# Optimization experiments

Measured on AMD Instinct MI355X. Metric: run time of the kernel, lower is better.

## Reference

```python
import jax, jax.numpy as jnp
import numpy as np

N, E, F, C, K, H = 100000, 1600000, 64, 32, 8, 36


def setup_inputs() -> dict:
    key = jax.random.key(0)
    ks = jax.random.split(key, 24)
    s = 0.1
    inp = {
        "x": jax.random.normal(ks[0], (N, F), jnp.float32),
        "edge_index": jax.random.randint(ks[1], (2, E), 0, N, dtype=jnp.int32),
        # ChebConv conv1_1: K x [F, H] weights + bias
        "W1_1": jax.random.normal(ks[2], (K, F, H), jnp.float32) * s,
        "b1_1": jnp.zeros((H,), jnp.float32),
        "g1_1": jnp.ones((H,), jnp.float32),
        "be1_1": jnp.zeros((H,), jnp.float32),
        # ChebConv conv1_2: K x [H, H]
        "W1_2": jax.random.normal(ks[3], (K, H, H), jnp.float32) * s,
        "b1_2": jnp.zeros((H,), jnp.float32),
        "g1_2": jnp.ones((H,), jnp.float32),
        "be1_2": jnp.zeros((H,), jnp.float32),
        # GINConv MLP: Linear(F,H) -> ReLU -> Linear(H,H)
        "gin_w1": jax.random.normal(ks[4], (F, H), jnp.float32) * s,
        "gin_b1": jnp.zeros((H,), jnp.float32),
        "gin_w2": jax.random.normal(ks[5], (H, H), jnp.float32) * s,
        "gin_b2": jnp.zeros((H,), jnp.float32),
        "g2": jnp.ones((H,), jnp.float32),
        "be2": jnp.zeros((H,), jnp.float32),
        # conv4: ChebConv K=1 on concat(3H) -> C  (pure linear, no propagation)
        "W4": jax.random.normal(ks[6], (1, 3 * H, C), jnp.float32) * s,
        "b4": jnp.zeros((C,), jnp.float32),
    }
    return inp


def _spmm(w, src, dst, x, n):
    # out[i] = sum_{e: dst_e=i} w_e * x[src_e]
    return jax.ops.segment_sum(w[:, None] * x[src], dst, num_segments=n)


def _cheb(x, src, dst, w, Wk, b):
    # PyG ChebConv with sym norm, lambda_max=2: L_hat = -D^-1/2 A D^-1/2 (loop weight 0)
    n = x.shape[0]
    Kk = Wk.shape[0]
    Tx0 = x
    out = Tx0 @ Wk[0]
    if Kk > 1:
        Tx1 = _spmm(w, src, dst, Tx0, n)
        out = out + Tx1 @ Wk[1]
        for k in range(2, Kk):
            Tx2 = 2.0 * _spmm(w, src, dst, Tx1, n) - Tx0
            out = out + Tx2 @ Wk[k]
            Tx0, Tx1 = Tx1, Tx2
    return out + b


def _bn(x, g, b, eps=1e-5):
    m = jnp.mean(x, axis=0)
    v = jnp.mean(jnp.square(x - m), axis=0)  # biased var, training-mode BN
    return g * (x - m) * jax.lax.rsqrt(v + eps) + b


def reference(x, edge_index, W1_1, b1_1, g1_1, be1_1, W1_2, b1_2, g1_2, be1_2,
              gin_w1, gin_b1, gin_w2, gin_b2, g2, be2, W4, b4):
    src, dst = edge_index[0], edge_index[1]
    n = x.shape[0]
    deg = jax.ops.segment_sum(jnp.ones((src.shape[0],), x.dtype), src, num_segments=n)
    dis = jnp.where(deg > 0, jax.lax.rsqrt(jnp.maximum(deg, 1.0)), 0.0)
    w = -dis[src] * dis[dst]  # scaled Laplacian edge weights

    x1_1 = jax.nn.relu(_bn(_cheb(x, src, dst, w, W1_1, b1_1), g1_1, be1_1))
    x1_2 = jax.nn.relu(_bn(_cheb(x1_1, src, dst, w, W1_2, b1_2), g1_2, be1_2))

    # GINConv (eps=0): nn(x + sum_{j in N(i)} x_j)
    agg = jax.ops.segment_sum(x[src], dst, num_segments=n)
    h = x + agg
    gin = jax.nn.relu(h @ gin_w1 + gin_b1) @ gin_w2 + gin_b2
    x2 = _bn(jax.nn.relu(gin), g2, be2)

    x4 = jnp.concatenate((x1_1, x1_2, x2), axis=1)
    return x4 @ W4[0] + b4
```

## Files before the change

### kernel.cpp

```cpp
#include <hip/hip_runtime.h>

constexpr int N_NODES = 100000;
constexpr int N_EDGES = 1600000;
constexpr int NBK  = 391;
constexpr int NBLK = 640;
constexpr int CHUNK = 2500;
constexpr int LCNT = NBK * NBLK;
constexpr int SCAN_BLKS = (LCNT + 255) / 256;


__device__ __forceinline__ unsigned bf16pack(float a, float b) {
    unsigned ua = __float_as_uint(a), ub = __float_as_uint(b);
    ua += 0x7fffu + ((ua >> 16) & 1u);
    ub += 0x7fffu + ((ub >> 16) & 1u);
    return (ua >> 16) | (ub & 0xffff0000u);
}
__device__ __forceinline__ float bflo(unsigned p) { return __uint_as_float(p << 16); }
__device__ __forceinline__ float bfhi(unsigned p) { return __uint_as_float(p & 0xffff0000u); }


__global__ __launch_bounds__(256) void part_count_kernel(
    const int* __restrict__ ei, int* __restrict__ cntD, int* __restrict__ cntS) {
    __shared__ int hd[NBK], hs[NBK];
    int tid = threadIdx.x;
    for (int i = tid; i < NBK; i += 256) { hd[i] = 0; hs[i] = 0; }
    __syncthreads();
    int e0 = blockIdx.x * CHUNK;
    for (int e = e0 + tid; e < e0 + CHUNK; e += 256) {
        int s = ei[e], d = ei[N_EDGES + e];
        atomicAdd(&hs[s >> 8], 1);
        atomicAdd(&hd[d >> 8], 1);
    }
    __syncthreads();
    for (int i = tid; i < NBK; i += 256) {
        cntD[i * NBLK + blockIdx.x] = hd[i];
        cntS[i * NBLK + blockIdx.x] = hs[i];
    }
}

__global__ __launch_bounds__(256) void scanA_kernel(const int* __restrict__ in,
                                                    int* __restrict__ out,
                                                    int* __restrict__ bsum, int L) {
    __shared__ int sm[256];
    int i = blockIdx.x * 256 + threadIdx.x;
    int v = (i < L) ? in[i] : 0;
    sm[threadIdx.x] = v;
    __syncthreads();
    for (int off = 1; off < 256; off <<= 1) {
        int t = (threadIdx.x >= off) ? sm[threadIdx.x - off] : 0;
        __syncthreads();
        sm[threadIdx.x] += t;
        __syncthreads();
    }
    if (i < L) out[i] = sm[threadIdx.x] - v;
    if (threadIdx.x == 255) bsum[blockIdx.x] = sm[255];
}

__global__ __launch_bounds__(1024) void scanB_kernel(int* __restrict__ bsum, int nb) {
    __shared__ int sm[1024];
    int t = threadIdx.x;
    int v = (t < nb) ? bsum[t] : 0;
// ... 51 lines not shown
    if (node < N_NODES) dis[node] = cnt[tid] > 0 ? rsqrtf((float)cnt[tid]) : 0.f;
}

__global__ __launch_bounds__(256) void csr_kernel(const int2* __restrict__ edgepart,
                                                  const int* __restrict__ scanD,
                                                  const float* __restrict__ dis,
                                                  int* __restrict__ rp,
                                                  int2* __restrict__ csrw) {
    __shared__ int cnt[256];
    __shared__ int lofs[256];
    __shared__ float disl[256];
    int b = blockIdx.x, tid = threadIdx.x;
    int beg = scanD[b * NBLK];
    int end = (b + 1 < NBK) ? scanD[(b + 1) * NBLK] : N_EDGES;
    int node = b * 256 + tid;
    cnt[tid] = 0;
    disl[tid] = (node < N_NODES) ? dis[node] : 0.f;
    __syncthreads();
    for (int j = beg + tid; j < end; j += 256)
        atomicAdd(&cnt[edgepart[j].y & 255], 1);
    __syncthreads();
    int v = cnt[tid];
    lofs[tid] = v;
    __syncthreads();
    for (int off = 1; off < 256; off <<= 1) {
        int t = (tid >= off) ? lofs[tid - off] : 0;
        __syncthreads();
        lofs[tid] += t;
        __syncthreads();
    }
    int myexc = lofs[tid] - v;
    if (node < N_NODES) rp[node] = beg + myexc;
    if (b == NBK - 1 && tid == 0) rp[N_NODES] = N_EDGES;
    __syncthreads();
    lofs[tid] = myexc;
    cnt[tid] = 0;
    __syncthreads();
    for (int j = beg + tid; j < end; j += 256) {
        int2 e = edgepart[j];
        int dl = e.y & 255;
        int pos = beg + lofs[dl] + atomicAdd(&cnt[dl], 1);
        csrw[pos] = make_int2(e.x, __float_as_int(-dis[e.x] * disl[dl]));
    }
}

__global__ void pack_x_kernel(const float* __restrict__ x, uint2* __restrict__ xbf) {
    int i = blockIdx.x * blockDim.x + threadIdx.x;
    if (i >= N_NODES * 16) return;
    float4 v = ((const float4*)x)[i];
    xbf[i] = make_uint2(bf16pack(v.x, v.y), bf16pack(v.z, v.w));
}


template <int FI, int SCALE, bool HAS_B2, bool BN_A, bool FUSE_STATS, bool OUT_BF16, bool DUAL>
__global__ __launch_bounds__(256) void cheb_step_kernel(
    const int* __restrict__ rp, const int2* __restrict__ csrw,
    const uint2* __restrict__ INb, const uint2* __restrict__ B2b,
    const uint2* __restrict__ Ab, const float* __restrict__ W,
    const float* __restrict__ ss, void* __restrict__ OUT,
    unsigned long long* __restrict__ OUTB, float* __restrict__ partials) {
    constexpr int RU2 = FI / 4;
    __shared__ float Wl[FI * 36];
    __shared__ float Atile[28][FI + 1];
    __shared__ float ls[72];
    int tid = threadIdx.x;
    for (int i = tid; i < FI * 36; i += 252) Wl[i] = W[i];
    int r0 = blockIdx.x * 28;
    const long long* ab8 = (const long long*)Ab;
    for (int i = tid; i < 28 * RU2; i += 252) {
        int r = i / RU2, u = i % RU2;
        int row = r0 + r;
        long long av = (row < N_NODES)
            ? __builtin_nontemporal_load(ab8 + (size_t)row * RU2 + u) : 0LL;
        unsigned lo = (unsigned)av, hi = (unsigned)(av >> 32);
        float f0 = bflo(lo), f1 = bfhi(lo), f2 = bflo(hi), f3 = bfhi(hi);
        if (BN_A) {
            int f = u * 4;
            f0 = fmaxf(fmaf(ss[f + 0], f0, ss[36 + f + 0]), 0.f);
            f1 = fmaxf(fmaf(ss[f + 1], f1, ss[36 + f + 1]), 0.f);
            f2 = fmaxf(fmaf(ss[f + 2], f2, ss[36 + f + 2]), 0.f);
            f3 = fmaxf(fmaf(ss[f + 3], f3, ss[36 + f + 3]), 0.f);
        }
        Atile[r][u * 4 + 0] = f0; Atile[r][u * 4 + 1] = f1;
        Atile[r][u * 4 + 2] = f2; Atile[r][u * 4 + 3] = f3;
    }
    if (FUSE_STATS && tid < 72) ls[tid] = 0.f;
    __syncthreads();
    int r = tid / 9, c = tid % 9;
    int row = r0 + r;
    bool valid = row < N_NODES;
    float ax = 0, ay = 0, az = 0, aw = 0;
    float bx = 0, by = 0, bz = 0, bw = 0;
    float cx = 0, cy = 0, cz = 0, cw = 0;
    float dx = 0, dy = 0, dz = 0, dw = 0;
    if (SCALE != 0 && valid) {
        int beg = rp[row], end = rp[row + 1];
        int j = beg;
        for (; j + 7 < end; j += 8) {
            int2 e0 = csrw[j],     e1 = csrw[j + 1], e2 = csrw[j + 2], e3 = csrw[j + 3];
            int2 e4 = csrw[j + 4], e5 = csrw[j + 5], e6 = csrw[j + 6], e7 = csrw[j + 7];
            uint2 u0 = INb[(size_t)e0.x * 9 + c];
            uint2 u1 = INb[(size_t)e1.x * 9 + c];
            uint2 u2 = INb[(size_t)e2.x * 9 + c];
            uint2 u3 = INb[(size_t)e3.x * 9 + c];
            uint2 u4 = INb[(size_t)e4.x * 9 + c];
            uint2 u5 = INb[(size_t)e5.x * 9 + c];
            uint2 u6 = INb[(size_t)e6.x * 9 + c];
            uint2 u7 = INb[(size_t)e7.x * 9 + c];
            float w0 = __int_as_float(e0.y), w1 = __int_as_float(e1.y);
            float w2 = __int_as_float(e2.y), w3 = __int_as_float(e3.y);
            float w4 = __int_as_float(e4.y), w5 = __int_as_float(e5.y);
            float w6 = __int_as_float(e6.y), w7 = __int_as_float(e7.y);
            ax = fmaf(w0, bflo(u0.x), ax); ay = fmaf(w0, bfhi(u0.x), ay);
            az = fmaf(w0, bflo(u0.y), az); aw = fmaf(w0, bfhi(u0.y), aw);
            bx = fmaf(w1, bflo(u1.x), bx); by = fmaf(w1, bfhi(u1.x), by);
            bz = fmaf(w1, bflo(u1.y), bz); bw = fmaf(w1, bfhi(u1.y), bw);
            cx = fmaf(w2, bflo(u2.x), cx); cy = fmaf(w2, bfhi(u2.x), cy);
            cz = fmaf(w2, bflo(u2.y), cz); cw = fmaf(w2, bfhi(u2.y), cw);
            dx = fmaf(w3, bflo(u3.x), dx); dy = fmaf(w3, bfhi(u3.x), dy);
            dz = fmaf(w3, bflo(u3.y), dz); dw = fmaf(w3, bfhi(u3.y), dw);
            ax = fmaf(w4, bflo(u4.x), ax); ay = fmaf(w4, bfhi(u4.x), ay);
            az = fmaf(w4, bflo(u4.y), az); aw = fmaf(w4, bfhi(u4.y), aw);
            bx = fmaf(w5, bflo(u5.x), bx); by = fmaf(w5, bfhi(u5.x), by);
            bz = fmaf(w5, bflo(u5.y), bz); bw = fmaf(w5, bfhi(u5.y), bw);
            cx = fmaf(w6, bflo(u6.x), cx); cy = fmaf(w6, bfhi(u6.x), cy);
            cz = fmaf(w6, bflo(u6.y), cz); cw = fmaf(w6, bfhi(u6.y), cw);
            dx = fmaf(w7, bflo(u7.x), dx); dy = fmaf(w7, bfhi(u7.x), dy);
            dz = fmaf(w7, bflo(u7.y), dz); dw = fmaf(w7, bfhi(u7.y), dw);
        }
        for (; j < end; ++j) {
            int2 e = csrw[j];
            uint2 u = INb[(size_t)e.x * 9 + c];
            float w = __int_as_float(e.y);
            ax = fmaf(w, bflo(u.x), ax); ay = fmaf(w, bfhi(u.x), ay);
            az = fmaf(w, bflo(u.y), az); aw = fmaf(w, bfhi(u.y), aw);
        }
        ax += bx + cx + dx; ay += by + cy + dy;
        az += bz + cz + dz; aw += bw + cw + dw;
    }
    float px = 0, py = 0, pz = 0, pw = 0;
    const float4* Wl4 = (const float4*)Wl;
#pragma unroll 4
    for (int f = 0; f < FI; ++f) {
        float a = Atile[r][f];
        float4 wv = Wl4[f * 9 + c];
        px = fmaf(a, wv.x, px); py = fmaf(a, wv.y, py);
        pz = fmaf(a, wv.z, pz); pw = fmaf(a, wv.w, pw);
    }
    const float S = (float)SCALE;
    float4 o;
    o.x = fmaf(S, ax, px); o.y = fmaf(S, ay, py);
    o.z = fmaf(S, az, pz); o.w = fmaf(S, aw, pw);
    if (valid) {
        if (HAS_B2) {
            uint2 u = B2b[(size_t)row * 9 + c];
            o.x -= bflo(u.x); o.y -= bfhi(u.x);
            o.z -= bflo(u.y); o.w -= bfhi(u.y);
        }
        if (OUT_BF16) {
            unsigned long long pv = (unsigned long long)bf16pack(o.x, o.y)
                                  | ((unsigned long long)bf16pack(o.z, o.w) << 32);
            __builtin_nontemporal_store(pv, (unsigned long long*)OUT + (size_t)row * 9 + c);
        } else {
            ((float4*)OUT)[(size_t)row * 9 + c] = o;
        }
        if (DUAL) {
            unsigned long long pv = (unsigned long long)bf16pack(o.x, o.y)
                                  | ((unsigned long long)bf16pack(o.z, o.w) << 32);
            __builtin_nontemporal_store(pv, OUTB + (size_t)row * 9 + c);
        }
        if (FUSE_STATS) {
            atomicAdd(&ls[c * 4 + 0], o.x); atomicAdd(&ls[36 + c * 4 + 0], o.x * o.x);
            atomicAdd(&ls[c * 4 + 1], o.y); atomicAdd(&ls[36 + c * 4 + 1], o.y * o.y);
            atomicAdd(&ls[c * 4 + 2], o.z); atomicAdd(&ls[36 + c * 4 + 2], o.z * o.z);
            atomicAdd(&ls[c * 4 + 3], o.w); atomicAdd(&ls[36 + c * 4 + 3], o.w * o.w);
        }
    }
    if (FUSE_STATS) {
        __syncthreads();
        if (tid < 72) partials[blockIdx.x * 72 + tid] = ls[tid];
    }
}


__global__ __launch_bounds__(256) void gin_gather_kernel(
    const int* __restrict__ rp, const int2* __restrict__ csrw,
    const uint2* __restrict__ Yb, const float* __restrict__ b1,
    const float* __restrict__ w2, const float* __restrict__ b2,
    float* __restrict__ OUT, float* __restrict__ partials) {
    __shared__ float W2l[36 * 36];
    __shared__ float B1l[36], B2l[36];
    __shared__ float M1t[28][37];
    __shared__ float ls[72];
    int tid = threadIdx.x;
    for (int i = tid; i < 36 * 36; i += 252) W2l[i] = w2[i];
    if (tid < 36) { B1l[tid] = b1[tid]; B2l[tid] = b2[tid]; }
    if (tid < 72) ls[tid] = 0.f;
    __syncthreads();
    int r = tid / 9, c = tid % 9;
    int row = blockIdx.x * 28 + r;
    bool valid = row < N_NODES;
    float ax = 0, ay = 0, az = 0, aw = 0;
    float bx = 0, by = 0, bz = 0, bw = 0;
    float cx = 0, cy = 0, cz = 0, cw = 0;
    float dx = 0, dy = 0, dz = 0, dw = 0;
    if (valid) {
        uint2 us = Yb[(size_t)row * 9 + c];
        ax = bflo(us.x); ay = bfhi(us.x); az = bflo(us.y); aw = bfhi(us.y);
        int beg = rp[row], end = rp[row + 1];
        int j = beg;
        for (; j + 7 < end; j += 8) {
            int s0 = csrw[j].x,     s1 = csrw[j + 1].x, s2 = csrw[j + 2].x, s3 = csrw[j + 3].x;
            int s4 = csrw[j + 4].x, s5 = csrw[j + 5].x, s6 = csrw[j + 6].x, s7 = csrw[j + 7].x;
            uint2 u0 = Yb[(size_t)s0 * 9 + c];
            uint2 u1 = Yb[(size_t)s1 * 9 + c];
            uint2 u2 = Yb[(size_t)s2 * 9 + c];
            uint2 u3 = Yb[(size_t)s3 * 9 + c];
            uint2 u4 = Yb[(size_t)s4 * 9 + c];
            uint2 u5 = Yb[(size_t)s5 * 9 + c];
            uint2 u6 = Yb[(size_t)s6 * 9 + c];
            uint2 u7 = Yb[(size_t)s7 * 9 + c];
            ax += bflo(u0.x) + bflo(u4.x); ay += bfhi(u0.x) + bfhi(u4.x);
            az += bflo(u0.y) + bflo(u4.y); aw += bfhi(u0.y) + bfhi(u4.y);
            bx += bflo(u1.x) + bflo(u5.x); by += bfhi(u1.x) + bfhi(u5.x);
            bz += bflo(u1.y) + bflo(u5.y); bw += bfhi(u1.y) + bfhi(u5.y);
            cx += bflo(u2.x) + bflo(u6.x); cy += bfhi(u2.x) + bfhi(u6.x);
            cz += bflo(u2.y) + bflo(u6.y); cw += bfhi(u2.y) + bfhi(u6.y);
            dx += bflo(u3.x) + bflo(u7.x); dy += bfhi(u3.x) + bfhi(u7.x);
            dz += bflo(u3.y) + bflo(u7.y); dw += bfhi(u3.y) + bfhi(u7.y);
        }
        for (; j < end; ++j) {
            uint2 u = Yb[(size_t)csrw[j].x * 9 + c];
            ax += bflo(u.x); ay += bfhi(u.x);
            az += bflo(u.y); aw += bfhi(u.y);
        }
        ax += bx + cx + dx; ay += by + cy + dy;
        az += bz + cz + dz; aw += bw + cw + dw;
    }
    float m0 = fmaxf(ax + B1l[c * 4 + 0], 0.f);
    float m1 = fmaxf(ay + B1l[c * 4 + 1], 0.f);
    float m2 = fmaxf(az + B1l[c * 4 + 2], 0.f);
    float m3 = fmaxf(aw + B1l[c * 4 + 3], 0.f);
    M1t[r][c * 4 + 0] = m0; M1t[r][c * 4 + 1] = m1;
    M1t[r][c * 4 + 2] = m2; M1t[r][c * 4 + 3] = m3;
    __syncthreads();
    float o0 = B2l[c * 4 + 0], o1 = B2l[c * 4 + 1];
    float o2 = B2l[c * 4 + 2], o3 = B2l[c * 4 + 3];
    const float4* W2l4 = (const float4*)W2l;
#pragma unroll 4
    for (int f = 0; f < 36; ++f) {
        float a = M1t[r][f];
        float4 wv = W2l4[f * 9 + c];
        o0 = fmaf(a, wv.x, o0); o1 = fmaf(a, wv.y, o1);
        o2 = fmaf(a, wv.z, o2); o3 = fmaf(a, wv.w, o3);
    }
    o0 = fmaxf(o0, 0.f); o1 = fmaxf(o1, 0.f);
    o2 = fmaxf(o2, 0.f); o3 = fmaxf(o3, 0.f);
    if (valid) {
        float4 o = {o0, o1, o2, o3};
        ((float4*)OUT)[(size_t)row * 9 + c] = o;
        atomicAdd(&ls[c * 4 + 0], o0); atomicAdd(&ls[36 + c * 4 + 0], o0 * o0);
        atomicAdd(&ls[c * 4 + 1], o1); atomicAdd(&ls[36 + c * 4 + 1], o1 * o1);
        atomicAdd(&ls[c * 4 + 2], o2); atomicAdd(&ls[36 + c * 4 + 2], o2 * o2);
        atomicAdd(&ls[c * 4 + 3], o3); atomicAdd(&ls[36 + c * 4 + 3], o3 * o3);
    }
    __syncthreads();
    if (tid < 72) partials[blockIdx.x * 72 + tid] = ls[tid];
}


__global__ __launch_bounds__(256) void finalize_kernel(
    const float* __restrict__ partials, int nb, const float* __restrict__ g,
    const float* __restrict__ be, float* __restrict__ ss) {
    __shared__ float rs[256], rq[256];
    int c = blockIdx.x;
    int t = threadIdx.x;
    float s = 0.f, q = 0.f;
    for (int i = t; i < nb; i += 256) {
        s += partials[i * 72 + c];
        q += partials[i * 72 + c + 36];
    }
    rs[t] = s; rq[t] = q;
    __syncthreads();
    for (int off = 128; off > 0; off >>= 1) {
        if (t < off) { rs[t] += rs[t + off]; rq[t] += rq[t + off]; }
        __syncthreads();
    }
    if (t == 0) {
        float m = rs[0] / (float)N_NODES;
        float v = rq[0] / (float)N_NODES - m * m;
        float sc = g[c] * rsqrtf(v + 1e-5f);
        ss[c] = sc;
        ss[36 + c] = be[c] - m * sc;
    }
}


__global__ __launch_bounds__(256) void fused3_kernel(
    const float* __restrict__ X1, const float* __restrict__ ssA,
    const float* __restrict__ X2, const float* __restrict__ ssB,
    const float* __restrict__ X3, const float* __restrict__ ssC,
    const float* __restrict__ W, const float* __restrict__ b,
    float* __restrict__ out) {
    __shared__ float Wl[108 * 32];
    __shared__ float Al[32][109];
    int tid = threadIdx.x;
    for (int i = tid; i < 108 * 32; i += 256) Wl[i] = W[i];
    int r0 = blockIdx.x * 32;
    for (int i = tid; i < 32 * 108; i += 256) {
        int r = i / 108, f = i % 108;
        int row = r0 + r;
        float v = 0.f;
        if (row < N_NODES) {
            if (f < 36) {
                v = fmaxf(fmaf(ssA[f], X1[(size_t)row * 36 + f], ssA[36 + f]), 0.f);
            } else if (f < 72) {
                int ff = f - 36;
                v = fmaxf(fmaf(ssB[ff], X2[(size_t)row * 36 + ff], ssB[36 + ff]), 0.f);
            } else {
                int ff = f - 72;
                v = fmaf(ssC[ff], X3[(size_t)row * 36 + ff], ssC[36 + ff]);
            }
        }
        Al[r][f] = v;
    }
    __syncthreads();
    int r = tid >> 3, q = tid & 7;
    int row = r0 + r;
    if (row >= N_NODES) return;
    float acc[4];
#pragma unroll
    for (int j = 0; j < 4; ++j) acc[j] = b[q * 4 + j];
    for (int f = 0; f < 108; ++f) {
        float a = Al[r][f];
#pragma unroll
        for (int j = 0; j < 4; ++j)
            acc[j] = fmaf(a, Wl[f * 32 + q * 4 + j], acc[j]);
    }
#pragma unroll
    for (int j = 0; j < 4; ++j) out[(size_t)row * 32 + q * 4 + j] = acc[j];
}


extern "C" void kernel_launch(void* const* d_in, const int* in_sizes, int n_in,
                              void* d_out, int out_size, void* d_ws, size_t ws_size,
                              hipStream_t stream) {
    const float* x      = (const float*)d_in[0];
    const int*   ei     = (const int*)d_in[1];
    const float* W1_1   = (const float*)d_in[2];
    const float* g1_1   = (const float*)d_in[4];
    const float* be1_1  = (const float*)d_in[5];
    const float* W1_2   = (const float*)d_in[6];
    const float* g1_2   = (const float*)d_in[8];
    const float* be1_2  = (const float*)d_in[9];
    const float* gin_w1 = (const float*)d_in[10];
    const float* gin_b1 = (const float*)d_in[11];
    const float* gin_w2 = (const float*)d_in[12];
    const float* gin_b2 = (const float*)d_in[13];
    const float* g2     = (const float*)d_in[14];
    const float* be2    = (const float*)d_in[15];
    const float* W4     = (const float*)d_in[16];
    const float* b4     = (const float*)d_in[17];
    float* out = (float*)d_out;

    char* ws = (char*)d_ws;
    size_t off = 0;
    auto alloc = [&](size_t bytes) -> char* {
        char* p = ws + off;
        off = (off + bytes + 255) & ~(size_t)255;
        return p;
    };
    int*   cntD  = (int*)alloc((size_t)LCNT * 4);
    int*   cntS  = (int*)alloc((size_t)LCNT * 4);
    int*   bsum  = (int*)alloc(1024 * 4);
    int*   rp    = (int*)alloc((size_t)(N_NODES + 1) * 4);
    float* dis   = (float*)alloc((size_t)N_NODES * 4);
    int2*  edgepart = (int2*)alloc((size_t)N_EDGES * 8);
    int*   srcpart  = (int*)alloc((size_t)N_EDGES * 4);
    int2*  csrw  = (int2*)alloc((size_t)N_EDGES * 8);
    float* ssA   = (float*)alloc(72 * 4);
    float* ssB   = (float*)alloc(72 * 4);
    float* ssC   = (float*)alloc(72 * 4);
    float* partials = (float*)alloc((size_t)6250 * 72 * 4);
    constexpr size_t NB36 = (size_t)N_NODES * 36 * 4;
    constexpr size_t NBBF = (size_t)N_NODES * 72;
    uint2* xbf = (uint2*)alloc((size_t)N_NODES * 128);
    uint2* R0  = (uint2*)alloc(NBBF);
    uint2* R1  = (uint2*)alloc(NBBF);
    uint2* R2  = (uint2*)alloc(NBBF);
    uint2* X1b = (uint2*)alloc(NBBF);
    float* X1  = (float*)alloc(NB36);
    float* X2  = (float*)alloc(NB36);
    float* X3  = (float*)alloc(NB36);
    if (off > ws_size) return;

    part_count_kernel<<<NBLK, 256, 0, stream>>>(ei, cntD, cntS);
    scanA_kernel<<<SCAN_BLKS, 256, 0, stream>>>(cntD, cntD, bsum, LCNT);
    scanB_kernel<<<1, 1024, 0, stream>>>(bsum, SCAN_BLKS);
    scanC_kernel<<<SCAN_BLKS, 256, 0, stream>>>(cntD, bsum, LCNT);
    scanA_kernel<<<SCAN_BLKS, 256, 0, stream>>>(cntS, cntS, bsum, LCNT);
    scanB_kernel<<<1, 1024, 0, stream>>>(bsum, SCAN_BLKS);
    scanC_kernel<<<SCAN_BLKS, 256, 0, stream>>>(cntS, bsum, LCNT);
    part_scatter_kernel<<<NBLK, 256, 0, stream>>>(ei, cntD, cntS, edgepart, srcpart);
    deg_kernel<<<NBK, 256, 0, stream>>>(srcpart, cntS, dis);
    csr_kernel<<<NBK, 256, 0, stream>>>(edgepart, cntD, dis, rp, csrw);
    pack_x_kernel<<<(N_NODES * 16 + 255) / 256, 256, 0, stream>>>(x, xbf);

    const int STEP_BLKS = (N_NODES + 27) / 28;
    const int F3_BLKS   = (N_NODES + 31) / 32;

    cheb_step_kernel<64, 0, false, false, false, true, false><<<STEP_BLKS, 252, 0, stream>>>(
        rp, csrw, nullptr, nullptr, xbf, W1_1 + 7 * 2304, nullptr, R0, nullptr, nullptr);
    cheb_step_kernel<64, 2, false, false, false, true, false><<<STEP_BLKS, 252, 0, stream>>>(
        rp, csrw, R0, nullptr, xbf, W1_1 + 6 * 2304, nullptr, R1, nullptr, nullptr);
    cheb_step_kernel<64, 2, true, false, false, true, false><<<STEP_BLKS, 252, 0, stream>>>(
        rp, csrw, R1, R0, xbf, W1_1 + 5 * 2304, nullptr, R2, nullptr, nullptr);
    cheb_step_kernel<64, 2, true, false, false, true, false><<<STEP_BLKS, 252, 0, stream>>>(
        rp, csrw, R2, R1, xbf, W1_1 + 4 * 2304, nullptr, R0, nullptr, nullptr);
    cheb_step_kernel<64, 2, true, false, false, true, false><<<STEP_BLKS, 252, 0, stream>>>(
        rp, csrw, R0, R2, xbf, W1_1 + 3 * 2304, nullptr, R1, nullptr, nullptr);
    cheb_step_kernel<64, 2, true, false, false, true, false><<<STEP_BLKS, 252, 0, stream>>>(
        rp, csrw, R1, R0, xbf, W1_1 + 2 * 2304, nullptr, R2, nullptr, nullptr);
    cheb_step_kernel<64, 2, true, false, false, true, false><<<STEP_BLKS, 252, 0, stream>>>(
        rp, csrw, R2, R1, xbf, W1_1 + 1 * 2304, nullptr, R0, nullptr, nullptr);
    cheb_step_kernel<64, 1, true, false, true, false, true><<<STEP_BLKS, 252, 0, stream>>>(
        rp, csrw, R0, R2, xbf, W1_1 + 0 * 2304, nullptr, X1,
        (unsigned long long*)X1b, partials);
    finalize_kernel<<<36, 256, 0, stream>>>(partials, STEP_BLKS, g1_1, be1_1, ssA);

    cheb_step_kernel<36, 0, false, true, false, true, false><<<STEP_BLKS, 252, 0, stream>>>(
        rp, csrw, nullptr, nullptr, X1b, W1_2 + 7 * 1296, ssA, R0, nullptr, nullptr);
    cheb_step_kernel<36, 2, false, true, false, true, false><<<STEP_BLKS, 252, 0, stream>>>(
        rp, csrw, R0, nullptr, X1b, W1_2 + 6 * 1296, ssA, R1, nullptr, nullptr);
    cheb_step_kernel<36, 2, true, true, false, true, false><<<STEP_BLKS, 252, 0, stream>>>(
        rp, csrw, R1, R0, X1b, W1_2 + 5 * 1296, ssA, R2, nullptr, nullptr);
    cheb_step_kernel<36, 2, true, true, false, true, false><<<STEP_BLKS, 252, 0, stream>>>(
        rp, csrw, R2, R1, X1b, W1_2 + 4 * 1296, ssA, R0, nullptr, nullptr);
    cheb_step_kernel<36, 2, true, true, false, true, false><<<STEP_BLKS, 252, 0, stream>>>(
        rp, csrw, R0, R2, X1b, W1_2 + 3 * 1296, ssA, R1, nullptr, nullptr);
    cheb_step_kernel<36, 2, true, true, false, true, false><<<STEP_BLKS, 252, 0, stream>>>(
        rp, csrw, R1, R0, X1b, W1_2 + 2 * 1296, ssA, R2, nullptr, nullptr);
    cheb_step_kernel<36, 2, true, true, false, true, false><<<STEP_BLKS, 252, 0, stream>>>(
        rp, csrw, R2, R1, X1b, W1_2 + 1 * 1296, ssA, R0, nullptr, nullptr);
    cheb_step_kernel<36, 1, true, true, true, false, false><<<STEP_BLKS, 252, 0, stream>>>(
        rp, csrw, R0, R2, X1b, W1_2 + 0 * 1296, ssA, X2, nullptr, partials);
    finalize_kernel<<<36, 256, 0, stream>>>(partials, STEP_BLKS, g1_2, be1_2, ssB);

    cheb_step_kernel<64, 0, false, false, false, true, false><<<STEP_BLKS, 252, 0, stream>>>(
        rp, csrw, nullptr, nullptr, xbf, gin_w1, nullptr, R0, nullptr, nullptr);
    gin_gather_kernel<<<STEP_BLKS, 252, 0, stream>>>(rp, csrw, R0, gin_b1,
                                                     gin_w2, gin_b2, X3, partials);
    finalize_kernel<<<36, 256, 0, stream>>>(partials, STEP_BLKS, g2, be2, ssC);

    fused3_kernel<<<F3_BLKS, 256, 0, stream>>>(X1, ssA, X2, ssB, X3, ssC, W4, b4, out);
}
```

Baseline: 961.8 us.

## Precompute all Chebyshev projections and run feature-sliced gather steps

Splits each fused Chebyshev step into two parts. All eight projections X·W_k are computed up front, and the Clenshaw-style recurrence then runs as pure gather steps. Features are stored in three 12-wide slices (slice-major layout), so each gather pass touches a smaller working set that fits better in cache. The GIN MLP is split into a gather kernel with bias and ReLU followed by a projection kernel with fused stats. The cost is three times as many gather launches, each re-reading the CSR, plus an extra round trip to memory for the eight projection buffers.

```diff
diff --git a/kernel.cpp b/kernel.cpp
--- a/kernel.cpp
+++ b/kernel.cpp
@@ -7,6 +7,7 @@
 constexpr int CHUNK = 2500;
 constexpr int LCNT = NBK * NBLK;
 constexpr int SCAN_BLKS = (LCNT + 255) / 256;
+constexpr size_t NS3 = (size_t)N_NODES * 3;
 
 
 __device__ __forceinline__ unsigned bf16pack(float a, float b) {
@@ -164,13 +165,11 @@
 }
 
 
-template <int FI, int SCALE, bool HAS_B2, bool BN_A, bool FUSE_STATS, bool OUT_BF16, bool DUAL>
-__global__ __launch_bounds__(256) void cheb_step_kernel(
-    const int* __restrict__ rp, const int2* __restrict__ csrw,
-    const uint2* __restrict__ INb, const uint2* __restrict__ B2b,
+template <int FI, bool BN_A, bool BIAS_RELU, bool FUSE_STATS>
+__global__ __launch_bounds__(256) void proj_kernel(
     const uint2* __restrict__ Ab, const float* __restrict__ W,
-    const float* __restrict__ ss, void* __restrict__ OUT,
-    unsigned long long* __restrict__ OUTB, float* __restrict__ partials) {
+    const float* __restrict__ ss, const float* __restrict__ bias,
+    uint2* __restrict__ Yout, float* __restrict__ partials) {
     constexpr int RU2 = FI / 4;
     __shared__ float Wl[FI * 36];
     __shared__ float Atile[28][FI + 1];
@@ -182,8 +181,10 @@
     for (int i = tid; i < 28 * RU2; i += 252) {
         int r = i / RU2, u = i % RU2;
         int row = r0 + r;
-        long long av = (row < N_NODES)
-            ? __builtin_nontemporal_load(ab8 + (size_t)row * RU2 + u) : 0LL;
+        size_t idx;
+        if (FI == 64) idx = (size_t)row * 16 + u;
+        else          idx = (size_t)(u / 3) * NS3 + (size_t)row * 3 + (u % 3);
+        long long av = (row < N_NODES) ? __builtin_nontemporal_load(ab8 + idx) : 0LL;
         unsigned lo = (unsigned)av, hi = (unsigned)(av >> 32);
         float f0 = bflo(lo), f1 = bfhi(lo), f2 = bflo(hi), f3 = bfhi(hi);
         if (BN_A) {
@@ -200,56 +201,6 @@
     __syncthreads();
     int r = tid / 9, c = tid % 9;
     int row = r0 + r;
-    bool valid = row < N_NODES;
-    float ax = 0, ay = 0, az = 0, aw = 0;
-    float bx = 0, by = 0, bz = 0, bw = 0;
-    float cx = 0, cy = 0, cz = 0, cw = 0;
-    float dx = 0, dy = 0, dz = 0, dw = 0;
-    if (SCALE != 0 && valid) {
-        int beg = rp[row], end = rp[row + 1];
-        int j = beg;
-        for (; j + 7 < end; j += 8) {
-            int2 e0 = csrw[j],     e1 = csrw[j + 1], e2 = csrw[j + 2], e3 = csrw[j + 3];
-            int2 e4 = csrw[j + 4], e5 = csrw[j + 5], e6 = csrw[j + 6], e7 = csrw[j + 7];
-            uint2 u0 = INb[(size_t)e0.x * 9 + c];
-            uint2 u1 = INb[(size_t)e1.x * 9 + c];
-            uint2 u2 = INb[(size_t)e2.x * 9 + c];
-            uint2 u3 = INb[(size_t)e3.x * 9 + c];
-            uint2 u4 = INb[(size_t)e4.x * 9 + c];
-            uint2 u5 = INb[(size_t)e5.x * 9 + c];
-            uint2 u6 = INb[(size_t)e6.x * 9 + c];
-            uint2 u7 = INb[(size_t)e7.x * 9 + c];
-            float w0 = __int_as_float(e0.y), w1 = __int_as_float(e1.y);
-            float w2 = __int_as_float(e2.y), w3 = __int_as_float(e3.y);
-            float w4 = __int_as_float(e4.y), w5 = __int_as_float(e5.y);
-            float w6 = __int_as_float(e6.y), w7 = __int_as_float(e7.y);
-            ax = fmaf(w0, bflo(u0.x), ax); ay = fmaf(w0, bfhi(u0.x), ay);
-            az = fmaf(w0, bflo(u0.y), az); aw = fmaf(w0, bfhi(u0.y), aw);
-            bx = fmaf(w1, bflo(u1.x), bx); by = fmaf(w1, bfhi(u1.x), by);
-            bz = fmaf(w1, bflo(u1.y), bz); bw = fmaf(w1, bfhi(u1.y), bw);
-            cx = fmaf(w2, bflo(u2.x), cx); cy = fmaf(w2, bfhi(u2.x), cy);
-            cz = fmaf(w2, bflo(u2.y), cz); cw = fmaf(w2, bfhi(u2.y), cw);
-            dx = fmaf(w3, bflo(u3.x), dx); dy = fmaf(w3, bfhi(u3.x), dy);
-            dz = fmaf(w3, bflo(u3.y), dz); dw = fmaf(w3, bfhi(u3.y), dw);
-            ax = fmaf(w4, bflo(u4.x), ax); ay = fmaf(w4, bfhi(u4.x), ay);
-            az = fmaf(w4, bflo(u4.y), az); aw = fmaf(w4, bfhi(u4.y), aw);
-            bx = fmaf(w5, bflo(u5.x), bx); by = fmaf(w5, bfhi(u5.x), by);
-            bz = fmaf(w5, bflo(u5.y), bz); bw = fmaf(w5, bfhi(u5.y), bw);
-            cx = fmaf(w6, bflo(u6.x), cx); cy = fmaf(w6, bfhi(u6.x), cy);
-            cz = fmaf(w6, bflo(u6.y), cz); cw = fmaf(w6, bfhi(u6.y), cw);
-            dx = fmaf(w7, bflo(u7.x), dx); dy = fmaf(w7, bfhi(u7.x), dy);
-            dz = fmaf(w7, bflo(u7.y), dz); dw = fmaf(w7, bfhi(u7.y), dw);
-        }
-        for (; j < end; ++j) {
-            int2 e = csrw[j];
-            uint2 u = INb[(size_t)e.x * 9 + c];
-            float w = __int_as_float(e.y);
-            ax = fmaf(w, bflo(u.x), ax); ay = fmaf(w, bfhi(u.x), ay);
-            az = fmaf(w, bflo(u.y), az); aw = fmaf(w, bfhi(u.y), aw);
-        }
-        ax += bx + cx + dx; ay += by + cy + dy;
-        az += bz + cz + dz; aw += bw + cw + dw;
-    }
     float px = 0, py = 0, pz = 0, pw = 0;
     const float4* Wl4 = (const float4*)Wl;
 #pragma unroll 4
@@ -259,125 +210,141 @@
         px = fmaf(a, wv.x, px); py = fmaf(a, wv.y, py);
         pz = fmaf(a, wv.z, pz); pw = fmaf(a, wv.w, pw);
     }
-    const float S = (float)SCALE;
-    float4 o;
-    o.x = fmaf(S, ax, px); o.y = fmaf(S, ay, py);
-    o.z = fmaf(S, az, pz); o.w = fmaf(S, aw, pw);
+    if (BIAS_RELU) {
+        px = fmaxf(px + bias[c * 4 + 0], 0.f);
+        py = fmaxf(py + bias[c * 4 + 1], 0.f);
+        pz = fmaxf(pz + bias[c * 4 + 2], 0.f);
+        pw = fmaxf(pw + bias[c * 4 + 3], 0.f);
+    }
+    if (row < N_NODES) {
+        unsigned long long pv = (unsigned long long)bf16pack(px, py)
+                              | ((unsigned long long)bf16pack(pz, pw) << 32);
+        __builtin_nontemporal_store(
+            pv, (unsigned long long*)(Yout + (size_t)(c / 3) * NS3) + (size_t)row * 3 + (c % 3));
+        if (FUSE_STATS) {
+            atomicAdd(&ls[c * 4 + 0], px); atomicAdd(&ls[36 + c * 4 + 0], px * px);
+            atomicAdd(&ls[c * 4 + 1], py); atomicAdd(&ls[36 + c * 4 + 1], py * py);
+            atomicAdd(&ls[c * 4 + 2], pz); atomicAdd(&ls[36 + c * 4 + 2], pz * pz);
+            atomicAdd(&ls[c * 4 + 3], pw); atomicAdd(&ls[36 + c * 4 + 3], pw * pw);
+        }
+    }
+    if (FUSE_STATS) {
+        __syncthreads();
+        if (tid < 72) partials[(size_t)blockIdx.x * 72 + tid] = ls[tid];
+    }
+}
+
+
+template <int SCALE, bool WEIGHTED, bool HAS_B2, bool BIAS_RELU, bool FUSE_STATS>
+__global__ __launch_bounds__(256) void gstep_kernel(
+    const int* __restrict__ rp, const int2* __restrict__ csrw,
+    const uint2* __restrict__ INs, const uint2* __restrict__ Ys,
+    const uint2* __restrict__ B2s, const float* __restrict__ bias,
+    uint2* __restrict__ OUTs, float* __restrict__ partials, int s) {
+    __shared__ float ls[24];
+    int tid = threadIdx.x;
+    if (FUSE_STATS) { if (tid < 24) ls[tid] = 0.f; __syncthreads(); }
+    int r = tid / 3, c = tid % 3;
+    int row = blockIdx.x * 84 + r;
+    bool valid = row < N_NODES;
+    float ox = 0, oy = 0, oz = 0, ow = 0;
     if (valid) {
-        if (HAS_B2) {
-            uint2 u = B2b[(size_t)row * 9 + c];
-            o.x -= bflo(u.x); o.y -= bfhi(u.x);
-            o.z -= bflo(u.y); o.w -= bfhi(u.y);
-        }
-        if (OUT_BF16) {
-            unsigned long long pv = (unsigned long long)bf16pack(o.x, o.y)
-                                  | ((unsigned long long)bf16pack(o.z, o.w) << 32);
-            __builtin_nontemporal_store(pv, (unsigned long long*)OUT + (size_t)row * 9 + c);
-        } else {
-            ((float4*)OUT)[(size_t)row * 9 + c] = o;
-        }
-        if (DUAL) {
-            unsigned long long pv = (unsigned long long)bf16pack(o.x, o.y)
-                                  | ((unsigned long long)bf16pack(o.z, o.w) << 32);
-            __builtin_nontemporal_store(pv, OUTB + (size_t)row * 9 + c);
-        }
-        if (FUSE_STATS) {
-            atomicAdd(&ls[c * 4 + 0], o.x); atomicAdd(&ls[36 + c * 4 + 0], o.x * o.x);
-            atomicAdd(&ls[c * 4 + 1], o.y); atomicAdd(&ls[36 + c * 4 + 1], o.y * o.y);
-            atomicAdd(&ls[c * 4 + 2], o.z); atomicAdd(&ls[36 + c * 4 + 2], o.z * o.z);
-            atomicAdd(&ls[c * 4 + 3], o.w); atomicAdd(&ls[36 + c * 4 + 3], o.w * o.w);
-        }
-    }
-    if (FUSE_STATS) {
-        __syncthreads();
-        if (tid < 72) partials[blockIdx.x * 72 + tid] = ls[tid];
-    }
-}
-
-
-__global__ __launch_bounds__(256) void gin_gather_kernel(
-    const int* __restrict__ rp, const int2* __restrict__ csrw,
-    const uint2* __restrict__ Yb, const float* __restrict__ b1,
-    const float* __restrict__ w2, const float* __restrict__ b2,
-    float* __restrict__ OUT, float* __restrict__ partials) {
-    __shared__ float W2l[36 * 36];
-    __shared__ float B1l[36], B2l[36];
-    __shared__ float M1t[28][37];
-    __shared__ float ls[72];
-    int tid = threadIdx.x;
-    for (int i = tid; i < 36 * 36; i += 252) W2l[i] = w2[i];
-    if (tid < 36) { B1l[tid] = b1[tid]; B2l[tid] = b2[tid]; }
-    if (tid < 72) ls[tid] = 0.f;
-    __syncthreads();
-    int r = tid / 9, c = tid % 9;
-    int row = blockIdx.x * 28 + r;
-    bool valid = row < N_NODES;
-    float ax = 0, ay = 0, az = 0, aw = 0;
-    float bx = 0, by = 0, bz = 0, bw = 0;
-    float cx = 0, cy = 0, cz = 0, cw = 0;
-    float dx = 0, dy = 0, dz = 0, dw = 0;
-    if (valid) {
-        uint2 us = Yb[(size_t)row * 9 + c];
-        ax = bflo(us.x); ay = bfhi(us.x); az = bflo(us.y); aw = bfhi(us.y);
+        long long yv = __builtin_nontemporal_load((const long long*)Ys + (size_t)row * 3 + c);
+        float ax = 0, ay = 0, az = 0, aw = 0;
+        float bx = 0, by = 0, bz = 0, bw = 0;
+        float cx = 0, cy = 0, cz = 0, cw = 0;
+        float dx = 0, dy = 0, dz = 0, dw = 0;
         int beg = rp[row], end = rp[row + 1];
         int j = beg;
         for (; j + 7 < end; j += 8) {
-            int s0 = csrw[j].x,     s1 = csrw[j + 1].x, s2 = csrw[j + 2].x, s3 = csrw[j + 3].x;
-            int s4 = csrw[j + 4].x, s5 = csrw[j + 5].x, s6 = csrw[j + 6].x, s7 = csrw[j + 7].x;
-            uint2 u0 = Yb[(size_t)s0 * 9 + c];
-            uint2 u1 = Yb[(size_t)s1 * 9 + c];
-            uint2 u2 = Yb[(size_t)s2 * 9 + c];
-            uint2 u3 = Yb[(size_t)s3 * 9 + c];
-            uint2 u4 = Yb[(size_t)s4 * 9 + c];
-            uint2 u5 = Yb[(size_t)s5 * 9 + c];
-            uint2 u6 = Yb[(size_t)s6 * 9 + c];
-            uint2 u7 = Yb[(size_t)s7 * 9 + c];
-            ax += bflo(u0.x) + bflo(u4.x); ay += bfhi(u0.x) + bfhi(u4.x);
-            az += bflo(u0.y) + bflo(u4.y); aw += bfhi(u0.y) + bfhi(u4.y);
-            bx += bflo(u1.x) + bflo(u5.x); by += bfhi(u1.x) + bfhi(u5.x);
-            bz += bflo(u1.y) + bflo(u5.y); bw += bfhi(u1.y) + bfhi(u5.y);
-            cx += bflo(u2.x) + bflo(u6.x); cy += bfhi(u2.x) + bfhi(u6.x);
-            cz += bflo(u2.y) + bflo(u6.y); cw += bfhi(u2.y) + bfhi(u6.y);
-            dx += bflo(u3.x) + bflo(u7.x); dy += bfhi(u3.x) + bfhi(u7.x);
-            dz += bflo(u3.y) + bflo(u7.y); dw += bfhi(u3.y) + bfhi(u7.y);
+            int2 e0 = csrw[j],     e1 = csrw[j + 1], e2 = csrw[j + 2], e3 = csrw[j + 3];
+            int2 e4 = csrw[j + 4], e5 = csrw[j + 5], e6 = csrw[j + 6], e7 = csrw[j + 7];
+            uint2 u0 = INs[(size_t)e0.x * 3 + c];
+            uint2 u1 = INs[(size_t)e1.x * 3 + c];
+            uint2 u2 = INs[(size_t)e2.x * 3 + c];
+            uint2 u3 = INs[(size_t)e3.x * 3 + c];
+            uint2 u4 = INs[(size_t)e4.x * 3 + c];
+            uint2 u5 = INs[(size_t)e5.x * 3 + c];
+            uint2 u6 = INs[(size_t)e6.x * 3 + c];
+            uint2 u7 = INs[(size_t)e7.x * 3 + c];
+            if (WEIGHTED) {
+                float w0 = __int_as_float(e0.y), w1 = __int_as_float(e1.y);
+                float w2 = __int_as_float(e2.y), w3 = __int_as_float(e3.y);
+                float w4 = __int_as_float(e4.y), w5 = __int_as_float(e5.y);
+                float w6 = __int_as_float(e6.y), w7 = __int_as_float(e7.y);
+                ax = fmaf(w0, bflo(u0.x), ax); ay = fmaf(w0, bfhi(u0.x), ay);
+                az = fmaf(w0, bflo(u0.y), az); aw = fmaf(w0, bfhi(u0.y), aw);
+                bx = fmaf(w1, bflo(u1.x), bx); by = fmaf(w1, bfhi(u1.x), by);
+                bz = fmaf(w1, bflo(u1.y), bz); bw = fmaf(w1, bfhi(u1.y), bw);
+                cx = fmaf(w2, bflo(u2.x), cx); cy = fmaf(w2, bfhi(u2.x), cy);
+                cz = fmaf(w2, bflo(u2.y), cz); cw = fmaf(w2, bfhi(u2.y), cw);
+                dx = fmaf(w3, bflo(u3.x), dx); dy = fmaf(w3, bfhi(u3.x), dy);
+                dz = fmaf(w3, bflo(u3.y), dz); dw = fmaf(w3, bfhi(u3.y), dw);
+                ax = fmaf(w4, bflo(u4.x), ax); ay = fmaf(w4, bfhi(u4.x), ay);
+                az = fmaf(w4, bflo(u4.y), az); aw = fmaf(w4, bfhi(u4.y), aw);
+                bx = fmaf(w5, bflo(u5.x), bx); by = fmaf(w5, bfhi(u5.x), by);
+                bz = fmaf(w5, bflo(u5.y), bz); bw = fmaf(w5, bfhi(u5.y), bw);
+                cx = fmaf(w6, bflo(u6.x), cx); cy = fmaf(w6, bfhi(u6.x), cy);
+                cz = fmaf(w6, bflo(u6.y), cz); cw = fmaf(w6, bfhi(u6.y), cw);
+                dx = fmaf(w7, bflo(u7.x), dx); dy = fmaf(w7, bfhi(u7.x), dy);
+                dz = fmaf(w7, bflo(u7.y), dz); dw = fmaf(w7, bfhi(u7.y), dw);
+            } else {
+                ax += bflo(u0.x) + bflo(u4.x); ay += bfhi(u0.x) + bfhi(u4.x);
+                az += bflo(u0.y) + bflo(u4.y); aw += bfhi(u0.y) + bfhi(u4.y);
+                bx += bflo(u1.x) + bflo(u5.x); by += bfhi(u1.x) + bfhi(u5.x);
+                bz += bflo(u1.y) + bflo(u5.y); bw += bfhi(u1.y) + bfhi(u5.y);
+                cx += bflo(u2.x) + bflo(u6.x); cy += bfhi(u2.x) + bfhi(u6.x);
+                cz += bflo(u2.y) + bflo(u6.y); cw += bfhi(u2.y) + bfhi(u6.y);
+                dx += bflo(u3.x) + bflo(u7.x); dy += bfhi(u3.x) + bfhi(u7.x);
+                dz += bflo(u3.y) + bflo(u7.y); dw += bfhi(u3.y) + bfhi(u7.y);
+            }
         }
         for (; j < end; ++j) {
-            uint2 u = Yb[(size_t)csrw[j].x * 9 + c];
-            ax += bflo(u.x); ay += bfhi(u.x);
-            az += bflo(u.y); aw += bfhi(u.y);
+            int2 e = csrw[j];
+            uint2 u = INs[(size_t)e.x * 3 + c];
+            if (WEIGHTED) {
+                float w = __int_as_float(e.y);
+                ax = fmaf(w, bflo(u.x), ax); ay = fmaf(w, bfhi(u.x), ay);
+                az = fmaf(w, bflo(u.y), az); aw = fmaf(w, bfhi(u.y), aw);
+            } else {
+                ax += bflo(u.x); ay += bfhi(u.x);
+                az += bflo(u.y); aw += bfhi(u.y);
+            }
         }
         ax += bx + cx + dx; ay += by + cy + dy;
         az += bz + cz + dz; aw += bw + cw + dw;
-    }
-    float m0 = fmaxf(ax + B1l[c * 4 + 0], 0.f);
-    float m1 = fmaxf(ay + B1l[c * 4 + 1], 0.f);
-    float m2 = fmaxf(az + B1l[c * 4 + 2], 0.f);
-    float m3 = fmaxf(aw + B1l[c * 4 + 3], 0.f);
-    M1t[r][c * 4 + 0] = m0; M1t[r][c * 4 + 1] = m1;
-    M1t[r][c * 4 + 2] = m2; M1t[r][c * 4 + 3] = m3;
-    __syncthreads();
-    float o0 = B2l[c * 4 + 0], o1 = B2l[c * 4 + 1];
-    float o2 = B2l[c * 4 + 2], o3 = B2l[c * 4 + 3];
-    const float4* W2l4 = (const float4*)W2l;
-#pragma unroll 4
-    for (int f = 0; f < 36; ++f) {
-        float a = M1t[r][f];
-        float4 wv = W2l4[f * 9 + c];
-        o0 = fmaf(a, wv.x, o0); o1 = fmaf(a, wv.y, o1);
-        o2 = fmaf(a, wv.z, o2); o3 = fmaf(a, wv.w, o3);
-    }
-    o0 = fmaxf(o0, 0.f); o1 = fmaxf(o1, 0.f);
-    o2 = fmaxf(o2, 0.f); o3 = fmaxf(o3, 0.f);
-    if (valid) {
-        float4 o = {o0, o1, o2, o3};
-        ((float4*)OUT)[(size_t)row * 9 + c] = o;
-        atomicAdd(&ls[c * 4 + 0], o0); atomicAdd(&ls[36 + c * 4 + 0], o0 * o0);
-        atomicAdd(&ls[c * 4 + 1], o1); atomicAdd(&ls[36 + c * 4 + 1], o1 * o1);
-        atomicAdd(&ls[c * 4 + 2], o2); atomicAdd(&ls[36 + c * 4 + 2], o2 * o2);
-        atomicAdd(&ls[c * 4 + 3], o3); atomicAdd(&ls[36 + c * 4 + 3], o3 * o3);
-    }
-    __syncthreads();
-    if (tid < 72) partials[blockIdx.x * 72 + tid] = ls[tid];
+        const float S = (float)SCALE;
+        unsigned ylo = (unsigned)yv, yhi = (unsigned)(yv >> 32);
+        ox = fmaf(S, ax, bflo(ylo)); oy = fmaf(S, ay, bfhi(ylo));
+        oz = fmaf(S, az, bflo(yhi)); ow = fmaf(S, aw, bfhi(yhi));
+        if (HAS_B2) {
+            long long bv = __builtin_nontemporal_load((const long long*)B2s + (size_t)row * 3 + c);
+            unsigned blo = (unsigned)bv, bhi = (unsigned)(bv >> 32);
+            ox -= bflo(blo); oy -= bfhi(blo);
+            oz -= bflo(bhi); ow -= bfhi(bhi);
+        }
+        if (BIAS_RELU) {
+            int cb = s * 12 + c * 4;
+            ox = fmaxf(ox + bias[cb + 0], 0.f); oy = fmaxf(oy + bias[cb + 1], 0.f);
+            oz = fmaxf(oz + bias[cb + 2], 0.f); ow = fmaxf(ow + bias[cb + 3], 0.f);
+        }
+        unsigned long long pv = (unsigned long long)bf16pack(ox, oy)
+                              | ((unsigned long long)bf16pack(oz, ow) << 32);
+        __builtin_nontemporal_store(pv, (unsigned long long*)OUTs + (size_t)row * 3 + c);
+        if (FUSE_STATS) {
+            atomicAdd(&ls[c * 4 + 0], ox); atomicAdd(&ls[12 + c * 4 + 0], ox * ox);
+            atomicAdd(&ls[c * 4 + 1], oy); atomicAdd(&ls[12 + c * 4 + 1], oy * oy);
+            atomicAdd(&ls[c * 4 + 2], oz); atomicAdd(&ls[12 + c * 4 + 2], oz * oz);
+            atomicAdd(&ls[c * 4 + 3], ow); atomicAdd(&ls[12 + c * 4 + 3], ow * ow);
+        }
+    }
+    if (FUSE_STATS) {
+        __syncthreads();
+        if (tid < 12) {
+            partials[(size_t)blockIdx.x * 72 + s * 12 + tid] = ls[tid];
+            partials[(size_t)blockIdx.x * 72 + 36 + s * 12 + tid] = ls[12 + tid];
+        }
+    }
 }
 
 
@@ -389,8 +356,8 @@
     int t = threadIdx.x;
     float s = 0.f, q = 0.f;
     for (int i = t; i < nb; i += 256) {
-        s += partials[i * 72 + c];
-        q += partials[i * 72 + c + 36];
+        s += partials[(size_t)i * 72 + c];
+        q += partials[(size_t)i * 72 + c + 36];
     }
     rs[t] = s; rq[t] = q;
     __syncthreads();
@@ -409,9 +376,9 @@
 
 
 __global__ __launch_bounds__(256) void fused3_kernel(
-    const float* __restrict__ X1, const float* __restrict__ ssA,
-    const float* __restrict__ X2, const float* __restrict__ ssB,
-    const float* __restrict__ X3, const float* __restrict__ ssC,
+    const uint2* __restrict__ X1b, const float* __restrict__ ssA,
+    const uint2* __restrict__ X2b, const float* __restrict__ ssB,
+    const uint2* __restrict__ X3b, const float* __restrict__ ssC,
     const float* __restrict__ W, const float* __restrict__ b,
     float* __restrict__ out) {
     __shared__ float Wl[108 * 32];
@@ -424,15 +391,13 @@
         int row = r0 + r;
         float v = 0.f;
         if (row < N_NODES) {
-            if (f < 36) {
-                v = fmaxf(fmaf(ssA[f], X1[(size_t)row * 36 + f], ssA[36 + f]), 0.f);
-            } else if (f < 72) {
-                int ff = f - 36;
-                v = fmaxf(fmaf(ssB[ff], X2[(size_t)row * 36 + ff], ssB[36 + ff]), 0.f);
-            } else {
-                int ff = f - 72;
-                v = fmaf(ssC[ff], X3[(size_t)row * 36 + ff], ssC[36 + ff]);
-            }
+            int t = f / 36, ff = f % 36, sl = ff / 12, w = ff % 12;
+            const uint2* base = (t == 0 ? X1b : (t == 1 ? X2b : X3b)) + (size_t)sl * NS3;
+            unsigned short u16 = ((const unsigned short*)base)[(size_t)row * 12 + w];
+            float xv = __uint_as_float((unsigned)u16 << 16);
+            if (t == 0)      v = fmaxf(fmaf(ssA[ff], xv, ssA[36 + ff]), 0.f);
+            else if (t == 1) v = fmaxf(fmaf(ssB[ff], xv, ssB[36 + ff]), 0.f);
+            else             v = fmaf(ssC[ff], xv, ssC[36 + ff]);
         }
         Al[r][f] = v;
     }
@@ -482,29 +447,32 @@
         off = (off + bytes + 255) & ~(size_t)255;
         return p;
     };
-    int*   cntD  = (int*)alloc((size_t)LCNT * 4);
-    int*   cntS  = (int*)alloc((size_t)LCNT * 4);
-    int*   bsum  = (int*)alloc(1024 * 4);
+    constexpr size_t SLICE_B = NS3 * 8;
+    constexpr size_t BUF36_B = SLICE_B * 3;
     int*   rp    = (int*)alloc((size_t)(N_NODES + 1) * 4);
-    float* dis   = (float*)alloc((size_t)N_NODES * 4);
-    int2*  edgepart = (int2*)alloc((size_t)N_EDGES * 8);
-    int*   srcpart  = (int*)alloc((size_t)N_EDGES * 4);
     int2*  csrw  = (int2*)alloc((size_t)N_EDGES * 8);
+    float* partials = (float*)alloc((size_t)4096 * 72 * 4);
     float* ssA   = (float*)alloc(72 * 4);
     float* ssB   = (float*)alloc(72 * 4);
     float* ssC   = (float*)alloc(72 * 4);
-    float* partials = (float*)alloc((size_t)6250 * 72 * 4);
-    constexpr size_t NB36 = (size_t)N_NODES * 36 * 4;
-    constexpr size_t NBBF = (size_t)N_NODES * 72;
-    uint2* xbf = (uint2*)alloc((size_t)N_NODES * 128);
-    uint2* R0  = (uint2*)alloc(NBBF);
-    uint2* R1  = (uint2*)alloc(NBBF);
-    uint2* R2  = (uint2*)alloc(NBBF);
-    uint2* X1b = (uint2*)alloc(NBBF);
-    float* X1  = (float*)alloc(NB36);
-    float* X2  = (float*)alloc(NB36);
-    float* X3  = (float*)alloc(NB36);
+    uint2* xbf   = (uint2*)alloc((size_t)N_NODES * 128);
+    char*  U     = alloc(8 * BUF36_B);
+    uint2* R0    = (uint2*)alloc(BUF36_B);
+    uint2* R1    = (uint2*)alloc(BUF36_B);
+    uint2* R2    = (uint2*)alloc(BUF36_B);
+    uint2* X1b   = (uint2*)alloc(BUF36_B);
+    uint2* X2b   = (uint2*)alloc(BUF36_B);
+    uint2* X3b   = (uint2*)alloc(BUF36_B);
+    uint2* m1b   = (uint2*)alloc(BUF36_B);
     if (off > ws_size) return;
+
+    int*   cntD = (int*)U;
+    int*   cntS = cntD + LCNT;
+    int*   bsum = cntS + LCNT;
+    float* dis  = (float*)(bsum + 1024);
+    int2*  edgepart = (int2*)(dis + N_NODES);
+    int*   srcpart  = (int*)(edgepart + N_EDGES);
+    uint2* Yall = (uint2*)U;
 
     part_count_kernel<<<NBLK, 256, 0, stream>>>(ei, cntD, cntS);
     scanA_kernel<<<SCAN_BLKS, 256, 0, stream>>>(cntD, cntD, bsum, LCNT);
@@ -518,51 +486,63 @@
     csr_kernel<<<NBK, 256, 0, stream>>>(edgepart, cntD, dis, rp, csrw);
     pack_x_kernel<<<(N_NODES * 16 + 255) / 256, 256, 0, stream>>>(x, xbf);
 
-    const int STEP_BLKS = (N_NODES + 27) / 28;
-    const int F3_BLKS   = (N_NODES + 31) / 32;
-
-    cheb_step_kernel<64, 0, false, false, false, true, false><<<STEP_BLKS, 252, 0, stream>>>(
-        rp, csrw, nullptr, nullptr, xbf, W1_1 + 7 * 2304, nullptr, R0, nullptr, nullptr);
-    cheb_step_kernel<64, 2, false, false, false, true, false><<<STEP_BLKS, 252, 0, stream>>>(
-        rp, csrw, R0, nullptr, xbf, W1_1 + 6 * 2304, nullptr, R1, nullptr, nullptr);
-    cheb_step_kernel<64, 2, true, false, false, true, false><<<STEP_BLKS, 252, 0, stream>>>(
-        rp, csrw, R1, R0, xbf, W1_1 + 5 * 2304, nullptr, R2, nullptr, nullptr);
-    cheb_step_kernel<64, 2, true, false, false, true, false><<<STEP_BLKS, 252, 0, stream>>>(
-        rp, csrw, R2, R1, xbf, W1_1 + 4 * 2304, nullptr, R0, nullptr, nullptr);
-    cheb_step_kernel<64, 2, true, false, false, true, false><<<STEP_BLKS, 252, 0, stream>>>(
-        rp, csrw, R0, R2, xbf, W1_1 + 3 * 2304, nullptr, R1, nullptr, nullptr);
-    cheb_step_kernel<64, 2, true, false, false, true, false><<<STEP_BLKS, 252, 0, stream>>>(
-        rp, csrw, R1, R0, xbf, W1_1 + 2 * 2304, nullptr, R2, nullptr, nullptr);
-    cheb_step_kernel<64, 2, true, false, false, true, false><<<STEP_BLKS, 252, 0, stream>>>(
-        rp, csrw, R2, R1, xbf, W1_1 + 1 * 2304, nullptr, R0, nullptr, nullptr);
-    cheb_step_kernel<64, 1, true, false, true, false, true><<<STEP_BLKS, 252, 0, stream>>>(
-        rp, csrw, R0, R2, xbf, W1_1 + 0 * 2304, nullptr, X1,
-        (unsigned long long*)X1b, partials);
-    finalize_kernel<<<36, 256, 0, stream>>>(partials, STEP_BLKS, g1_1, be1_1, ssA);
-
-    cheb_step_kernel<36, 0, false, true, false, true, false><<<STEP_BLKS, 252, 0, stream>>>(
-        rp, csrw, nullptr, nullptr, X1b, W1_2 + 7 * 1296, ssA, R0, nullptr, nullptr);
-    cheb_step_kernel<36, 2, false, true, false, true, false><<<STEP_BLKS, 252, 0, stream>>>(
-        rp, csrw, R0, nullptr, X1b, W1_2 + 6 * 1296, ssA, R1, nullptr, nullptr);
-    cheb_step_kernel<36, 2, true, true, false, true, false><<<STEP_BLKS, 252, 0, stream>>>(
-        rp, csrw, R1, R0, X1b, W1_2 + 5 * 1296, ssA, R2, nullptr, nullptr);
-    cheb_step_kernel<36, 2, true, true, false, true, false><<<STEP_BLKS, 252, 0, stream>>>(
-        rp, csrw, R2, R1, X1b, W1_2 + 4 * 1296, ssA, R0, nullptr, nullptr);
-    cheb_step_kernel<36, 2, true, true, false, true, false><<<STEP_BLKS, 252, 0, stream>>>(
-        rp, csrw, R0, R2, X1b, W1_2 + 3 * 1296, ssA, R1, nullptr, nullptr);
-    cheb_step_kernel<36, 2, true, true, false, true, false><<<STEP_BLKS, 252, 0, stream>>>(
-        rp, csrw, R1, R0, X1b, W1_2 + 2 * 1296, ssA, R2, nullptr, nullptr);
-    cheb_step_kernel<36, 2, true, true, false, true, false><<<STEP_BLKS, 252, 0, stream>>>(
-        rp, csrw, R2, R1, X1b, W1_2 + 1 * 1296, ssA, R0, nullptr, nullptr);
-    cheb_step_kernel<36, 1, true, true, true, false, false><<<STEP_BLKS, 252, 0, stream>>>(
-        rp, csrw, R0, R2, X1b, W1_2 + 0 * 1296, ssA, X2, nullptr, partials);
-    finalize_kernel<<<36, 256, 0, stream>>>(partials, STEP_BLKS, g1_2, be1_2, ssB);
-
-    cheb_step_kernel<64, 0, false, false, false, true, false><<<STEP_BLKS, 252, 0, stream>>>(
-        rp, csrw, nullptr, nullptr, xbf, gin_w1, nullptr, R0, nullptr, nullptr);
-    gin_gather_kernel<<<STEP_BLKS, 252, 0, stream>>>(rp, csrw, R0, gin_b1,
-                                                     gin_w2, gin_b2, X3, partials);
-    finalize_kernel<<<36, 256, 0, stream>>>(partials, STEP_BLKS, g2, be2, ssC);
-
-    fused3_kernel<<<F3_BLKS, 256, 0, stream>>>(X1, ssA, X2, ssB, X3, ssC, W4, b4, out);
-}
+    const int PBLKS = (N_NODES + 27) / 28;
+    const int GBLKS = (N_NODES + 83) / 84;
+    const int F3_BLKS = (N_NODES + 31) / 32;
+
+    auto Y  = [&](int k) { return Yall + (size_t)k * (NS3 * 3); };
+    auto SL = [&](uint2* base, int s) { return base + (size_t)s * NS3; };
+
+    for (int k = 7; k >= 0; --k)
+        proj_kernel<64, false, false, false><<<PBLKS, 252, 0, stream>>>(
+            xbf, W1_1 + k * 2304, nullptr, nullptr, Y(k), nullptr);
+    for (int s = 0; s < 3; ++s) {
+        gstep_kernel<2, true, false, false, false><<<GBLKS, 252, 0, stream>>>(
+            rp, csrw, SL(Y(7), s), SL(Y(6), s), nullptr, nullptr, SL(R0, s), nullptr, s);
+        gstep_kernel<2, true, true, false, false><<<GBLKS, 252, 0, stream>>>(
+            rp, csrw, SL(R0, s), SL(Y(5), s), SL(Y(7), s), nullptr, SL(R1, s), nullptr, s);
+        gstep_kernel<2, true, true, false, false><<<GBLKS, 252, 0, stream>>>(
+            rp, csrw, SL(R1, s), SL(Y(4), s), SL(R0, s), nullptr, SL(R2, s), nullptr, s);
+        gstep_kernel<2, true, true, false, false><<<GBLKS, 252, 0, stream>>>(
+            rp, csrw, SL(R2, s), SL(Y(3), s), SL(R1, s), nullptr, SL(R0, s), nullptr, s);
+        gstep_kernel<2, true, true, false, false><<<GBLKS, 252, 0, stream>>>(
+            rp, csrw, SL(R0, s), SL(Y(2), s), SL(R2, s), nullptr, SL(R1, s), nullptr, s);
+        gstep_kernel<2, true, true, false, false><<<GBLKS, 252, 0, stream>>>(
+            rp, csrw, SL(R1, s), SL(Y(1), s), SL(R0, s), nullptr, SL(R2, s), nullptr, s);
+        gstep_kernel<1, true, true, false, true><<<GBLKS, 252, 0, stream>>>(
+            rp, csrw, SL(R2, s), SL(Y(0), s), SL(R1, s), nullptr, SL(X1b, s), partials, s);
+    }
+    finalize_kernel<<<36, 256, 0, stream>>>(partials, GBLKS, g1_1, be1_1, ssA);
+
+    for (int k = 7; k >= 0; --k)
+        proj_kernel<36, true, false, false><<<PBLKS, 252, 0, stream>>>(
+            X1b, W1_2 + k * 1296, ssA, nullptr, Y(k), nullptr);
+    for (int s = 0; s < 3; ++s) {
+        gstep_kernel<2, true, false, false, false><<<GBLKS, 252, 0, stream>>>(
+            rp, csrw, SL(Y(7), s), SL(Y(6), s), nullptr, nullptr, SL(R0, s), nullptr, s);
+        gstep_kernel<2, true, true, false, false><<<GBLKS, 252, 0, stream>>>(
+            rp, csrw, SL(R0, s), SL(Y(5), s), SL(Y(7), s), nullptr, SL(R1, s), nullptr, s);
+        gstep_kernel<2, true, true, false, false><<<GBLKS, 252, 0, stream>>>(
+            rp, csrw, SL(R1, s), SL(Y(4), s), SL(R0, s), nullptr, SL(R2, s), nullptr, s);
+        gstep_kernel<2, true, true, false, false><<<GBLKS, 252, 0, stream>>>(
+            rp, csrw, SL(R2, s), SL(Y(3), s), SL(R1, s), nullptr, SL(R0, s), nullptr, s);
+        gstep_kernel<2, true, true, false, false><<<GBLKS, 252, 0, stream>>>(
+            rp, csrw, SL(R0, s), SL(Y(2), s), SL(R2, s), nullptr, SL(R1, s), nullptr, s);
+        gstep_kernel<2, true, true, false, false><<<GBLKS, 252, 0, stream>>>(
+            rp, csrw, SL(R1, s), SL(Y(1), s), SL(R0, s), nullptr, SL(R2, s), nullptr, s);
+        gstep_kernel<1, true, true, false, true><<<GBLKS, 252, 0, stream>>>(
+            rp, csrw, SL(R2, s), SL(Y(0), s), SL(R1, s), nullptr, SL(X2b, s), partials, s);
+    }
+    finalize_kernel<<<36, 256, 0, stream>>>(partials, GBLKS, g1_2, be1_2, ssB);
+
+    proj_kernel<64, false, false, false><<<PBLKS, 252, 0, stream>>>(
+        xbf, gin_w1, nullptr, nullptr, Y(0), nullptr);
+    for (int s = 0; s < 3; ++s)
+        gstep_kernel<1, false, false, true, false><<<GBLKS, 252, 0, stream>>>(
+            rp, csrw, SL(Y(0), s), SL(Y(0), s), nullptr, gin_b1, SL(m1b, s), nullptr, s);
+    proj_kernel<36, false, true, true><<<PBLKS, 252, 0, stream>>>(
+        m1b, gin_w2, nullptr, gin_b2, X3b, partials);
+    finalize_kernel<<<36, 256, 0, stream>>>(partials, PBLKS, g2, be2, ssC);
+
+    fused3_kernel<<<F3_BLKS, 256, 0, stream>>>(X1b, ssA, X2b, ssB, X3b, ssC, W4, b4, out);
+}
```

New measurement: 1.355 ms. 40.9% more time.
